# Kernel tuning notes

Hardware: AMD Instinct MI355X
Metric: run time of the kernel (lower is better)

## Reference

```python
import jax, jax.numpy as jnp
import numpy as np

DIM = 64   # model dim == d_inner (expand=1)
Hh = 64
Ww = 64
BATCH = 4
D_IN = 64
N_ST = 8   # d_state
DT_R = 4   # dt_rank = ceil(dim/16)
K = 4      # depthwise conv kernel
NB = 8     # total CrossMambaBlocks: 4 (depth=1) + 4 final cross blocks


def setup_inputs():
    key = jax.random.key(0)
    ks = iter(jax.random.split(key, 40))
    def rn(shape, s=0.02):
        return jax.random.normal(next(ks), shape, jnp.float32) * s
    A_init = jnp.log(jnp.tile(jnp.arange(1, N_ST + 1, dtype=jnp.float32), (NB, D_IN, 1)))
    return dict(
        img1=rn((BATCH, DIM, Hh, Ww), 1.0), img2=rn((BATCH, DIM, Hh, Ww), 1.0),
        img1_sum=rn((BATCH, DIM, Hh, Ww), 1.0), img2_sum=rn((BATCH, DIM, Hh, Ww), 1.0),
        norm0_w=jnp.ones((NB, DIM)), norm0_b=jnp.zeros((NB, DIM)),
        norm1_w=jnp.ones((NB, DIM)), norm1_b=jnp.zeros((NB, DIM)),
        in_w=rn((NB, 2 * D_IN, DIM)), in_b=jnp.zeros((NB, 2 * D_IN)),
        conv_w_f=rn((NB, D_IN, 1, K), 0.1), conv_b_f=jnp.zeros((NB, D_IN)),
        conv_w_b=rn((NB, D_IN, 1, K), 0.1), conv_b_b=jnp.zeros((NB, D_IN)),
        xproj_w_f=rn((NB, DT_R + 2 * N_ST, D_IN)), xproj_w_b=rn((NB, DT_R + 2 * N_ST, D_IN)),
        dtproj_w_f=rn((NB, D_IN, DT_R), 0.1), dtproj_b_f=jnp.zeros((NB, D_IN)),
        dtproj_w_b=rn((NB, D_IN, DT_R), 0.1), dtproj_b_b=jnp.zeros((NB, D_IN)),
        A_log_f=A_init, A_log_b=A_init,
        D_f=jnp.ones((NB, D_IN)), D_b=jnp.ones((NB, D_IN)),
        ln_w=jnp.ones((NB, D_IN)), ln_b=jnp.zeros((NB, D_IN)),
        mout_w=rn((NB, DIM, D_IN)), mout_b=jnp.zeros((NB, DIM)),
        fop_w=rn((DIM, 2 * DIM)), fop_b=jnp.zeros((DIM,)),
    )


def _ln(x, w, b):
    m = x.mean(-1, keepdims=True)
    v = ((x - m) ** 2).mean(-1, keepdims=True)
    return (x - m) * jax.lax.rsqrt(v + 1e-5) * w + b


def _dwconv(x, w, b):
    # x: [b,L,d], w: [d,1,K] depthwise causal conv along L
    y = jax.lax.conv_general_dilated(
        x.transpose(0, 2, 1), w, (1,), [(K - 1, 0)],
        dimension_numbers=('NCH', 'OIH', 'NCH'),
        feature_group_count=x.shape[-1])
    return y.transpose(0, 2, 1) + b


def _ssm(u, dt, Bm, Cm, A, Dm):
    # u,dt: [b,L,d]; Bm,Cm: [b,L,n]; A: [d,n]; Dm: [d]
    dA = jnp.exp(dt[..., None] * A)                 # [b,L,d,n]
    dBu = (dt * u)[..., None] * Bm[:, :, None, :]   # [b,L,d,n]
    def step(h, xs):
        dA_t, dBu_t, C_t = xs
        h = dA_t * h + dBu_t
        return h, jnp.einsum('bdn,bn->bd', h, C_t)
    h0 = jnp.zeros(u.shape[:1] + A.shape, u.dtype)
    _, ys = jax.lax.scan(step, h0, (jnp.moveaxis(dA, 1, 0), jnp.moveaxis(dBu, 1, 0), jnp.moveaxis(Cm, 1, 0)))
    return jnp.moveaxis(ys, 0, 1) + u * Dm


def _direction(x_in, extra, conv_w, conv_b, xproj_w, dtproj_w, dtproj_b, A_log, Dm, flip):
    if flip:
        x_in = x_in[:, ::-1]
        extra = extra[:, ::-1]
    u = jax.nn.silu(_dwconv(x_in, conv_w, conv_b))
    dbl = jnp.einsum('bld,ed->ble', extra, xproj_w)     # cross: dt/B/C from extra embedding
    dtr = dbl[..., :DT_R]
    Bm = dbl[..., DT_R:DT_R + N_ST]
    Cm = dbl[..., DT_R + N_ST:]
    dt = jax.nn.softplus(jnp.einsum('blr,dr->bld', dtr, dtproj_w) + dtproj_b)
    y = _ssm(u, dt, Bm, Cm, -jnp.exp(A_log), Dm)
    if flip:
        y = y[:, ::-1]
    return y


def _cross_block(i, x, extra, p):
    skip = x
    x = _ln(x, p['norm0_w'][i], p['norm0_b'][i])
    extra = _ln(extra, p['norm1_w'][i], p['norm1_b'][i])
    xz = jnp.einsum('bld,ed->ble', x, p['in_w'][i]) + p['in_b'][i]
    x_in, z = xz[..., :D_IN], xz[..., D_IN:]
    y_f = _direction(x_in, extra, p['conv_w_f'][i], p['conv_b_f'][i], p['xproj_w_f'][i],
                     p['dtproj_w_f'][i], p['dtproj_b_f'][i], p['A_log_f'][i], p['D_f'][i], False)
    y_b = _direction(x_in, extra, p['conv_w_b'][i], p['conv_b_b'][i], p['xproj_w_b'][i],
                     p['dtproj_w_b'][i], p['dtproj_b_b'][i], p['A_log_b'][i], p['D_b'][i], True)
    y = 0.5 * (y_f + y_b)                    # if_devide_out=True
    y = _ln(y, p['ln_w'][i], p['ln_b'][i])   # use_norm=True
    y = y * jax.nn.silu(z)
    out = jnp.einsum('bld,ed->ble', y, p['mout_w'][i]) + p['mout_b'][i]
    return out + skip


def _forward(img1, img2, img1_sum, img2_sum, norm0_w, norm0_b, norm1_w, norm1_b, in_w, in_b,
             conv_w_f, conv_b_f, conv_w_b, conv_b_b, xproj_w_f, xproj_w_b,
             dtproj_w_f, dtproj_b_f, dtproj_w_b, dtproj_b_b, A_log_f, A_log_b,
             D_f, D_b, ln_w, ln_b, mout_w, mout_b, fop_w, fop_b):
    p = dict(norm0_w=norm0_w, norm0_b=norm0_b, norm1_w=norm1_w, norm1_b=norm1_b,
             in_w=in_w, in_b=in_b, conv_w_f=conv_w_f, conv_b_f=conv_b_f,
             conv_w_b=conv_w_b, conv_b_b=conv_b_b, xproj_w_f=xproj_w_f, xproj_w_b=xproj_w_b,
             dtproj_w_f=dtproj_w_f, dtproj_b_f=dtproj_b_f, dtproj_w_b=dtproj_w_b,
             dtproj_b_b=dtproj_b_b, A_log_f=A_log_f, A_log_b=A_log_b, D_f=D_f, D_b=D_b,
             ln_w=ln_w, ln_b=ln_b, mout_w=mout_w, mout_b=mout_b)
    def seq(t):
        b, c, h, w = t.shape
        return t.reshape(b, c, h * w).transpose(0, 2, 1)   # b (h w) c
    s1, s2, s1s, s2s = seq(img1), seq(img2), seq(img1_sum), seq(img2_sum)
    # depth=1 cross-fusion loop
    s1 = _cross_block(0, s1, s1s, p)
    s2 = _cross_block(1, s2, s2s, p)
    s1s = _cross_block(2, s1s, s1, p)
    s2s = _cross_block(3, s2s, s2, p)
    # final cross blocks
    i1l = _cross_block(4, s1, s2, p)
    i1g = _cross_block(5, s1, s2s, p)
    i2l = _cross_block(6, s2, s1, p)
    i2g = _cross_block(7, s2, s1s, p)
    c1 = jnp.concatenate([i1l, i1g], -1)
    c2 = jnp.concatenate([i2l, i2g], -1)
    fusion = jnp.einsum('ble,ce->blc', 0.5 * (c1 + c2), fop_w) + fop_b
    b = img1.shape[0]
    return fusion.transpose(0, 2, 1).reshape(b, DIM, Hh, Ww)


def reference(img1, img2, img1_sum, img2_sum, norm0_w, norm0_b, norm1_w, norm1_b, in_w, in_b,
              conv_w_f, conv_b_f, conv_w_b, conv_b_b, xproj_w_f, xproj_w_b,
              dtproj_w_f, dtproj_b_f, dtproj_w_b, dtproj_b_b, A_log_f, A_log_b,
              D_f, D_b, ln_w, ln_b, mout_w, mout_b, fop_w, fop_b):
    return _forward(img1, img2, img1_sum, img2_sum, norm0_w, norm0_b, norm1_w, norm1_b, in_w, in_b,
                    conv_w_f, conv_b_f, conv_w_b, conv_b_b, xproj_w_f, xproj_w_b,
                    dtproj_w_f, dtproj_b_f, dtproj_w_b, dtproj_b_b, A_log_f, A_log_b,
                    D_f, D_b, ln_w, ln_b, mout_w, mout_b, fop_w, fop_b)
```

## Files before the change

kernel.cpp:

```cpp
#include <hip/hip_runtime.h>
#include <hip/hip_bf16.h>

#define BX 4
#define LX 4096
#define DX 64
#define NX 8
#define TCH 16
#define NCH 256
#define BLD (BX*LX*DX)

typedef unsigned short u16;
typedef __attribute__((ext_vector_type(8))) short v8s;
typedef __attribute__((ext_vector_type(4))) float v4f;

#define L2E 1.44269504088896f
#define LN2 0.69314718055994531f

__device__ __forceinline__ float b2f(u16 u){ return __uint_as_float(((unsigned)u)<<16); }
__device__ __forceinline__ u16 f2b(float f){
  unsigned u = __float_as_uint(f);
  unsigned r = (u + 0x7FFFu + ((u>>16)&1u)) >> 16;
  return (u16)r;
}
__device__ __forceinline__ float siluf(float x){
  return x * __builtin_amdgcn_rcpf(1.f + __builtin_amdgcn_exp2f(-x*L2E));
}
__device__ __forceinline__ float softplusf(float x){
  const float t = __builtin_amdgcn_exp2f(-fabsf(x)*L2E);
  return fmaxf(x, 0.f) + LN2 * __builtin_amdgcn_logf(1.f + t);
}

__device__ __forceinline__ v4f mfma16(v8s a, v8s b, v4f c){
  return __builtin_amdgcn_mfma_f32_16x16x32_bf16(a, b, c, 0, 0, 0);
}
__device__ __forceinline__ void split8(const float* v, v8s& hi, v8s& lo){
  #pragma unroll
  for(int j=0;j<8;j++){
    const short h = (short)f2b(v[j]);
    hi[j] = h;
    lo[j] = (short)f2b(v[j] - b2f((u16)h));
  }
}
__device__ __forceinline__ void afrag(const float* tile, int lane, int k0, v8s& hi, v8s& lo){
  const float* p = tile + (lane&15)*72 + k0 + ((lane>>4)<<3);
  float v[8];
  const float4 a = *(const float4*)(p);
  const float4 b = *(const float4*)(p+4);
  v[0]=a.x; v[1]=a.y; v[2]=a.z; v[3]=a.w;
  v[4]=b.x; v[5]=b.y; v[6]=b.z; v[7]=b.w;
  split8(v, hi, lo);
}

struct Ctx {
  const float *nw0,*nb0,*nw1,*nb1;
  const float *inb;
  const float *convw,*convb;
  const float *dtw,*dtb;
  const float *A2,*Dp;
  const float *lnw,*lnb;
  const float *moutb;
  const float *fopb;
  const u16 *wih,*wil,*wxh,*wxl,*wmh,*wml,*wfh,*wfl;
  float *act[4], *outc[4];
  float *xin[4], *zz[4], *dbl[4], *Pp[4], *qq[4], *hin[4];
};

struct BlkDesc { int i; const float* x; const float* e; float* out; int slot; };
struct StageArgs { BlkDesc d[4]; };

struct PrepEnt { const void* src; float* dst; int n; int mode; };
struct PrepAll { PrepEnt a[21]; };
struct WPrep { const void* sA; const void* sB; u16* dh; u16* dl; long off; int E; int KS; int kind; int i; };
struct WPrepAll { WPrep a[25]; };

__global__ __launch_bounds__(256) void k_prep(PrepAll pa, WPrepAll wa, const u16* df){
  const bool isbf = (df[0] == 0x3F80u);
  if(blockIdx.y < 21){
    PrepEnt p = pa.a[blockIdx.y];
    int idx = blockIdx.x*256 + threadIdx.x;
    if(idx < p.n){
      float v = isbf ? b2f(((const u16*)p.src)[idx]) : ((const float*)p.src)[idx];
      if(p.mode==2) v = -__expf(v) * L2E;
      p.dst[idx] = v;
    }
  } else {
    WPrep p = wa.a[blockIdx.y - 21];
    const int wv = threadIdx.x >> 6, lane = threadIdx.x & 63;
    const int idx = blockIdx.x*4 + wv;
    const int NT = (p.E + 15) >> 4;
    if(idx >= NT*p.KS) return;
    const int ct = idx / p.KS, ks = idx % p.KS;
    const int g  = ct*16 + (lane & 15);
    const int k0 = ks*32 + ((lane>>4)<<3);
    const int K  = p.KS*32;
    bool valid; long si = 0; const void* sp = p.sA;
    if(p.kind == 1){
      valid = (g < 40);
      const int dir = g/20, e = g - dir*20;
      if(dir) sp = p.sB;
      si = ((long)p.i*20 + e)*64 + k0;
    } else {
      valid = (g < p.E);
      si = p.off + (long)g*K + k0;
    }
    float v[8];
    #pragma unroll
    for(int j2=0;j2<8;j2++){
      float x = 0.f;
      if(valid) x = isbf ? b2f(((const u16*)sp)[si+j2]) : ((const float*)sp)[si+j2];
      v[j2] = x;
    }
    v8s hi, lo; split8(v, hi, lo);
    const size_t o = ((size_t)idx*64 + lane)*8;
    *(v8s*)(p.dh + o) = hi;
    *(v8s*)(p.dl + o) = lo;
  }
}

struct SeqArgs { const void* src[4]; };

__global__ __launch_bounds__(256) void k_seq(SeqArgs s, Ctx c, const u16* df){
  const bool isbf = (df[0] == 0x3F80u);
  __shared__ float ld[64*65];
  const int t = blockIdx.z, b = blockIdx.y, l0 = blockIdx.x*64;
  float* dst = c.act[t];
  const int tx = threadIdx.x, ty = threadIdx.y;
  if(isbf){
    const u16* src = (const u16*)s.src[t];
    #pragma unroll
    for(int k=0;k<16;k++){ int d = k*4+ty; ld[d*65+tx] = b2f(src[(size_t)(b*64+d)*LX + l0+tx]); }
  } else {
    const float* src = (const float*)s.src[t];
    #pragma unroll
    for(int k=0;k<16;k++){ int d = k*4+ty; ld[d*65+tx] = src[(size_t)(b*64+d)*LX + l0+tx]; }
  }
  __syncthreads();
  #pragma unroll
  for(int k=0;k<16;k++){ int p = k*4+ty; dst[(size_t)(b*LX + l0+p)*64 + tx] = ld[tx*65+p]; }
}

__device__ __forceinline__ void coop72(float* sb, const float* g, int t){
  #pragma unroll
  for(int k=0;k<4;k++){
    const int idx = k*256 + t;
    const int row = idx >> 4;
    const int c4  = (idx & 15) << 2;
    *(float4*)(sb + row*72 + c4) = *(const float4*)(g + (size_t)row*64 + c4);
  }
}
__device__ __forceinline__ void coop72_avg(float* sb, const float* g0, const float* g1, int t){
  #pragma unroll
  for(int k=0;k<4;k++){
    const int idx = k*256 + t;
    const int row = idx >> 4;
    const int c4  = (idx & 15) << 2;
    const float4 a = *(const float4*)(g0 + (size_t)row*64 + c4);
    const float4 b = *(const float4*)(g1 + (size_t)row*64 + c4);
    float4 o; o.x=0.5f*(a.x+b.x); o.y=0.5f*(a.y+b.y); o.z=0.5f*(a.z+b.z); o.w=0.5f*(a.w+b.w);
    *(float4*)(sb + row*72 + c4) = o;
  }
}

__device__ __forceinline__ void ln72(float* sb, int lane, const float* w, const float* b){
  float r[64];
  float* p = sb + lane*72;
  #pragma unroll
  for(int cc=0;cc<64;cc+=4){ float4 v = *(const float4*)(p+cc); r[cc]=v.x; r[cc+1]=v.y; r[cc+2]=v.z; r[cc+3]=v.w; }
  float m=0.f;
  #pragma unroll
  for(int d=0;d<64;d++) m += r[d];
  m *= (1.f/64.f);
  float va=0.f;
  #pragma unroll
  for(int d=0;d<64;d++){ float t=r[d]-m; va += t*t; }
  va *= (1.f/64.f);
  const float rs = rsqrtf(va + 1e-5f);
  #pragma unroll
  for(int d=0;d<64;d++) r[d] = (r[d]-m)*rs*w[d] + b[d];
  #pragma unroll
  for(int cc=0;cc<64;cc+=4){ float4 v={r[cc],r[cc+1],r[cc+2],r[cc+3]}; *(float4*)(p+cc)=v; }
}

__global__ __launch_bounds__(256) void k_front(Ctx c, StageArgs sa){
  __shared__ __align__(16) float sx[64*72];
  __shared__ __align__(16) float se[64*72];
  const BlkDesc bd = sa.d[blockIdx.y];
  const int i = bd.i;
  const int tile = blockIdx.x;
  const int b = tile >> 6;
  const int l0 = (tile & 63) << 6;
  const int bl0 = b*LX + l0;
  const int t = threadIdx.x;
  const int wave = t >> 6, lane = t & 63;

  coop72(sx, bd.x + (size_t)bl0*64, t);
  coop72(se, bd.e + (size_t)bl0*64, t);
  __syncthreads();
  if(wave == 0)      ln72(sx, lane, c.nw0 + i*64, c.nb0 + i*64);
  else if(wave == 1) ln72(se, lane, c.nw1 + i*64, c.nb1 + i*64);
  __syncthreads();

  const int m0 = wave*16;
  const int q  = lane >> 4;
  const int n15 = lane & 15;

  {
    v8s ah[2], al[2];
    afrag(sx + m0*72, lane, 0,  ah[0], al[0]);
    afrag(sx + m0*72, lane, 32, ah[1], al[1]);
    const v8s* WH = (const v8s*)c.wih + (size_t)i*1024;
    const v8s* WL = (const v8s*)c.wil + (size_t)i*1024;
    #pragma unroll 1
    for(int ct=0; ct<8; ct++){
      const int colg = ct*16 + n15;
      const float bias = c.inb[i*128 + colg];
      v4f acc = {bias, bias, bias, bias};
      #pragma unroll
      for(int ks=0; ks<2; ks++){
        const v8s wh = WH[(ct*2+ks)*64 + lane];
        const v8s wl = WL[(ct*2+ks)*64 + lane];
        acc = mfma16(ah[ks], wl, acc);
        acc = mfma16(al[ks], wh, acc);
        acc = mfma16(ah[ks], wh, acc);
      }
      float* baseo = (colg < 64) ? c.xin[bd.slot] : c.zz[bd.slot];
      const int col = colg & 63;
      #pragma unroll
      for(int r=0;r<4;r++){
        const int row = m0 + q*4 + r;
        baseo[(size_t)(bl0+row)*64 + col] = acc[r];
      }
    }
  }
  {
    v8s ah[2], al[2];
    afrag(se + m0*72, lane, 0,  ah[0], al[0]);
    afrag(se + m0*72, lane, 32, ah[1], al[1]);
    const v8s* WH = (const v8s*)c.wxh + (size_t)i*384;
    const v8s* WL = (const v8s*)c.wxl + (size_t)i*384;
    #pragma unroll 1
    for(int ct=0; ct<3; ct++){
      v4f acc = {0.f,0.f,0.f,0.f};
      #pragma unroll
      for(int ks=0; ks<2; ks++){
        const v8s wh = WH[(ct*2+ks)*64 + lane];
        const v8s wl = WL[(ct*2+ks)*64 + lane];
        acc = mfma16(ah[ks], wl, acc);
        acc = mfma16(al[ks], wh, acc);
        acc = mfma16(ah[ks], wh, acc);
      }
      const int g = ct*16 + n15;
      if(g < 40){
        const int dir = (g >= 20);
        const int e = g - dir*20;
        float* dp = c.dbl[bd.slot] + (size_t)dir*((size_t)BX*LX*20);
        #pragma unroll
        for(int r=0;r<4;r++){
          const int row = m0 + q*4 + r;
          dp[(size_t)(bl0+row)*20 + e] = acc[r];
        }
      }
    }
  }
}

template<int DIR>
__device__ __forceinline__ void scan1_dir(const float* xs, const float* meta,
    const float4 cwv, const float cbv, const float4 dwv, const float dtbv,
    const float* A2, float* h, float& S){
  #pragma unroll
  for(int t=0;t<TCH;t++){
    float w0,w1,w2,xc; int lr;
    if(DIR==0){ lr=t;       w0=xs[t];    w1=xs[t+1];  w2=xs[t+2];  xc=xs[t+3]; }
    else      { lr=15-t;    w0=xs[18-t]; w1=xs[17-t]; w2=xs[16-t]; xc=xs[15-t]; }
    const float u = siluf(cwv.x*w0 + cwv.y*w1 + cwv.z*w2 + cwv.w*xc + cbv);
    const float* m = meta + lr*20;
    const float4 m0 = *(const float4*)(m);
    const float dt = softplusf(m0.x*dwv.x + m0.y*dwv.y + m0.z*dwv.z + m0.w*dwv.w + dtbv);
    const float du = dt*u;
    const float4 mb0 = *(const float4*)(m+4);
    const float4 mb1 = *(const float4*)(m+8);
    const float Bv[8] = {mb0.x,mb0.y,mb0.z,mb0.w,mb1.x,mb1.y,mb1.z,mb1.w};
    #pragma unroll
    for(int n=0;n<8;n++){
      const float dA = __builtin_amdgcn_exp2f(dt*A2[n]);
      h[n] = dA*h[n] + du*Bv[n];
    }
    S += dt;
  }
}

__global__ __launch_bounds__(64) void k_scan1(Ctx c, StageArgs sa){
  __shared__ __align__(16) float meta[TCH*20];
  const int zid = blockIdx.z;
  const int j = zid >> 1, dir = zid & 1;
  const BlkDesc bd = sa.d[j];
  const int i = bd.i, slot = bd.slot;
  const int ch = blockIdx.x, b = blockIdx.y;
  const int d = threadIdx.x;
  const int pb = (dir*8 + i)*64 + d;

  const float4 cwv = *(const float4*)(c.convw + (size_t)pb*4);
  const float  cbv = c.convb[pb];
  const float4 dwv = *(const float4*)(c.dtw + (size_t)pb*4);
  const float  dtbv = c.dtb[pb];
  const float4 A2a = *(const float4*)(c.A2 + (size_t)pb*8);
  const float4 A2b = *(const float4*)(c.A2 + (size_t)pb*8 + 4);
  float A2[8] = {A2a.x,A2a.y,A2a.z,A2a.w,A2b.x,A2b.y,A2b.z,A2b.w};

  {
    const float4* s = (const float4*)(c.dbl[slot] + (size_t)dir*((size_t)BX*LX*20)
                                      + (size_t)(b*LX + ch*TCH)*20);
    float4* dst = (float4*)meta;
    #pragma unroll
    for(int k=0;k<2;k++){ int idx = k*64 + d; if(idx < 80) dst[idx] = s[idx]; }
  }
  __syncthreads();

  const int base = ch*TCH;
  const float* X = c.xin[slot] + (size_t)b*LX*64 + d;
  float xs[19];
  if(dir==0){
    #pragma unroll
    for(int k=0;k<19;k++){ const int r = base - 3 + k; xs[k] = (r>=0) ? X[(size_t)r*64] : 0.f; }
  } else {
    #pragma unroll
    for(int k=0;k<19;k++){ const int r = base + k; xs[k] = (r<LX) ? X[(size_t)r*64] : 0.f; }
  }

  float h[8];
  #pragma unroll
  for(int n=0;n<8;n++) h[n]=0.f;
  float S = 0.f;
  if(dir==0) scan1_dir<0>(xs, meta, cwv, cbv, dwv, dtbv, A2, h, S);
  else       scan1_dir<1>(xs, meta, cwv, cbv, dwv, dtbv, A2, h, S);

  float* Pw = c.Pp[slot] + (size_t)(dir*NCH + ch)*((size_t)BX*512) + (size_t)b*512 + d;
  float* Qw = c.qq[slot] + (size_t)(dir*NCH + ch)*((size_t)BX*512) + (size_t)b*512 + d;
  #pragma unroll
  for(int n=0;n<8;n++){
    Pw[n*64] = __builtin_amdgcn_exp2f(A2[n]*S);
    Qw[n*64] = h[n];
  }
}

__global__ __launch_bounds__(64) void k_mid(Ctx c, StageArgs sa){
  const int b = blockIdx.x >> 3;
  const int seg = blockIdx.x & 7;
  const int dir = blockIdx.y & 1, j = blockIdx.y >> 1;
  const BlkDesc bd = sa.d[j];
  const int slot = bd.slot;
  const int nd = seg*64 + threadIdx.x;
  const size_t base = (size_t)dir*NCH*((size_t)BX*512) + (size_t)b*512 + nd;
  const size_t STR = (size_t)BX*512;
  const float* P = c.Pp[slot] + base;
  const float* Q = c.qq[slot] + base;
  float* H = c.hin[slot] + base;
  float h = 0.f;
  float Pv[32], Qv[32];
  #pragma unroll 1
  for(int g=0; g<NCH/32; g++){
    #pragma unroll
    for(int k=0;k<32;k++){
      const int ch = dir ? (NCH-1 - (g*32+k)) : (g*32+k);
      Pv[k] = P[(size_t)ch*STR]; Qv[k] = Q[(size_t)ch*STR];
    }
    #pragma unroll
    for(int k=0;k<32;k++){
      const int ch = dir ? (NCH-1 - (g*32+k)) : (g*32+k);
      H[(size_t)ch*STR] = h;
      h = fmaf(Pv[k], h, Qv[k]);
    }
  }
}

__global__ __launch_bounds__(256) void k_back(Ctx c, StageArgs sa){
  __shared__ __align__(16) float sy[64*72];
  __shared__ __align__(16) float smeta[64*40];
  const BlkDesc bd = sa.d[blockIdx.y];
  const int i = bd.i, slot = bd.slot;
  const int tile = blockIdx.x;
  const int b = tile >> 6;
  const int l0 = (tile & 63) << 6;
  const int bl0 = b*LX + l0;
  const int t = threadIdx.x;
  const int wave = t >> 6, lane = t & 63;

  #pragma unroll
  for(int d2=0; d2<2; d2++){
    const float4* s = (const float4*)(c.dbl[slot] + (size_t)d2*((size_t)BX*LX*20) + (size_t)bl0*20);
    #pragma unroll
    for(int k=0;k<2;k++){
      const int idx = k*256 + t;
      if(idx < 320){
        const int row = idx/5, e4 = idx - row*5;
        *(float4*)(smeta + row*40 + d2*20 + e4*4) = s[idx];
      }
    }
  }
  __syncthreads();

  const int m0 = wave*16;
  {
    const int ch = (tile & 63)*4 + wave;
    const int d2 = lane;
    const float* X = c.xin[slot] + (size_t)b*LX*64 + d2;
    float xs[22];
    #pragma unroll
    for(int k=0;k<22;k++){
      const int r = l0 + m0 + k - 3;
      xs[k] = (r>=0 && r<LX) ? X[(size_t)r*64] : 0.f;
    }
    #pragma unroll
    for(int dir=0; dir<2; dir++){
      const int pb = (dir*8 + i)*64 + d2;
      const float4 cwv = *(const float4*)(c.convw + (size_t)pb*4);
      const float  cbv = c.convb[pb];
      const float4 dwv = *(const float4*)(c.dtw + (size_t)pb*4);
      const float  dtbv = c.dtb[pb];
      const float4 A2a = *(const float4*)(c.A2 + (size_t)pb*8);
      const float4 A2b = *(const float4*)(c.A2 + (size_t)pb*8 + 4);
      const float A2r[8] = {A2a.x,A2a.y,A2a.z,A2a.w,A2b.x,A2b.y,A2b.z,A2b.w};
      const float Dv = c.Dp[pb];
      float h[8];
      const float* hp = c.hin[slot] + (size_t)(dir*NCH + ch)*((size_t)BX*512) + (size_t)b*512 + d2;
      #pragma unroll
      for(int n=0;n<8;n++) h[n] = hp[n*64];
      #pragma unroll
      for(int k=0;k<16;k++){
        const int lr = dir ? (m0+15-k) : (m0+k);
        const float w0 = dir ? xs[21-k] : xs[k];
        const float w1 = dir ? xs[20-k] : xs[k+1];
        const float w2 = dir ? xs[19-k] : xs[k+2];
        const float xc = dir ? xs[18-k] : xs[k+3];
        const float u = siluf(cwv.x*w0 + cwv.y*w1 + cwv.z*w2 + cwv.w*xc + cbv);
        const float* m = smeta + lr*40 + dir*20;
        const float4 m0v = *(const float4*)(m);
        const float dt = softplusf(m0v.x*dwv.x + m0v.y*dwv.y + m0v.z*dwv.z + m0v.w*dwv.w + dtbv);
        const float du = dt*u;
        const float4 mb0 = *(const float4*)(m+4);
        const float4 mb1 = *(const float4*)(m+8);
        const float Bv[8] = {mb0.x,mb0.y,mb0.z,mb0.w,mb1.x,mb1.y,mb1.z,mb1.w};
        float yv = u*Dv;
        #pragma unroll
        for(int n=0;n<8;n++){
          const float dA = __builtin_amdgcn_exp2f(dt*A2r[n]);
          h[n] = dA*h[n] + du*Bv[n];
        }
        const float4 mc0 = *(const float4*)(m+12);
        const float4 mc1 = *(const float4*)(m+16);
        const float Cv[8] = {mc0.x,mc0.y,mc0.z,mc0.w,mc1.x,mc1.y,mc1.z,mc1.w};
        #pragma unroll
        for(int n=0;n<8;n++) yv += h[n]*Cv[n];
        if(dir==0) sy[lr*72 + d2] = 0.5f*yv;
        else       sy[lr*72 + d2] += 0.5f*yv;
      }
    }
  }
  __syncthreads();
  if(wave == 0){
    ln72(sy, lane, c.lnw + i*64, c.lnb + i*64);
    float* p = sy + lane*72;
    const float* zp = c.zz[slot] + (size_t)(bl0+lane)*64;
    #pragma unroll
    for(int d3=0;d3<64;d3++){ p[d3] *= siluf(zp[d3]); }
  }
  __syncthreads();

  const int q  = lane >> 4;
  const int n15 = lane & 15;
  v8s ah[2], al[2];
  afrag(sy + m0*72, lane, 0,  ah[0], al[0]);
  afrag(sy + m0*72, lane, 32, ah[1], al[1]);
  const v8s* WH = (const v8s*)c.wmh + (size_t)i*512;
  const v8s* WL = (const v8s*)c.wml + (size_t)i*512;
  #pragma unroll 1
  for(int ct=0; ct<4; ct++){
    const int col = ct*16 + n15;
    const float bias = c.moutb[i*64 + col];
    v4f acc = {bias, bias, bias, bias};
    #pragma unroll
    for(int ks=0; ks<2; ks++){
      const v8s wh = WH[(ct*2+ks)*64 + lane];
      const v8s wl = WL[(ct*2+ks)*64 + lane];
      acc = mfma16(ah[ks], wl, acc);
      acc = mfma16(al[ks], wh, acc);
      acc = mfma16(ah[ks], wh, acc);
    }
    #pragma unroll
    for(int r=0;r<4;r++){
      const int row = m0 + q*4 + r;
      bd.out[(size_t)(bl0+row)*64 + col] = acc[r] + bd.x[(size_t)(bl0+row)*64 + col];
    }
  }
}

__global__ __launch_bounds__(256) void k_fusion(Ctx c, void* outp, const u16* df){
  const bool isbf = (df[0] == 0x3F80u);
  __shared__ __align__(16) float sL[64*72];
  __shared__ __align__(16) float sH[64*72];
  __shared__ __align__(16) float sT[64*68];
  const int tile = blockIdx.x;
  const int b = tile >> 6;
  const int l0 = (tile & 63) << 6;
  const int bl0 = b*LX + l0;
  const int t = threadIdx.x;
  const int wave = t >> 6, lane = t & 63;

  coop72_avg(sL, c.outc[0] + (size_t)bl0*64, c.outc[2] + (size_t)bl0*64, t);
  coop72_avg(sH, c.outc[1] + (size_t)bl0*64, c.outc[3] + (size_t)bl0*64, t);
  __syncthreads();

  const int m0 = wave*16;
  const int q  = lane >> 4;
  const int n15 = lane & 15;
  v8s ah[4], al[4];
  afrag(sL + m0*72, lane, 0,  ah[0], al[0]);
  afrag(sL + m0*72, lane, 32, ah[1], al[1]);
  afrag(sH + m0*72, lane, 0,  ah[2], al[2]);
  afrag(sH + m0*72, lane, 32, ah[3], al[3]);
  const v8s* WH = (const v8s*)c.wfh;
  const v8s* WL = (const v8s*)c.wfl;
  #pragma unroll 1
  for(int ct=0; ct<4; ct++){
    const int col = ct*16 + n15;
    const float bias = c.fopb[col];
    v4f acc = {bias, bias, bias, bias};
    #pragma unroll
    for(int ks=0; ks<4; ks++){
      const v8s wh = WH[(ct*4+ks)*64 + lane];
      const v8s wl = WL[(ct*4+ks)*64 + lane];
      acc = mfma16(ah[ks], wl, acc);
      acc = mfma16(al[ks], wh, acc);
      acc = mfma16(ah[ks], wh, acc);
    }
    #pragma unroll
    for(int r=0;r<4;r++) sT[col*68 + m0 + q*4 + r] = acc[r];
  }
  __syncthreads();

  const int o  = t >> 2;
  const int p0 = (t & 3) * 16;
  float v[16];
  #pragma unroll
  for(int k=0;k<16;k+=4){
    const float4 x = *(const float4*)(sT + o*68 + p0 + k);
    v[k]=x.x; v[k+1]=x.y; v[k+2]=x.z; v[k+3]=x.w;
  }
  const size_t off = (size_t)(b*64+o)*LX + l0 + p0;
  if(isbf){
    u16 hb[16];
    #pragma unroll
    for(int k=0;k<16;k++) hb[k] = f2b(v[k]);
    uint4 u0, u1;
    u0.x = hb[0] | ((unsigned)hb[1]<<16);  u0.y = hb[2] | ((unsigned)hb[3]<<16);
    u0.z = hb[4] | ((unsigned)hb[5]<<16);  u0.w = hb[6] | ((unsigned)hb[7]<<16);
    u1.x = hb[8] | ((unsigned)hb[9]<<16);  u1.y = hb[10]| ((unsigned)hb[11]<<16);
    u1.z = hb[12]| ((unsigned)hb[13]<<16); u1.w = hb[14]| ((unsigned)hb[15]<<16);
    *(uint4*)((u16*)outp + off)     = u0;
    *(uint4*)((u16*)outp + off + 8) = u1;
  } else {
    float* fo = (float*)outp + off;
    #pragma unroll
    for(int k=0;k<16;k+=4){ float4 x={v[k],v[k+1],v[k+2],v[k+3]}; *(float4*)(fo+k)=x; }
  }
}

extern "C" void kernel_launch(void* const* d_in, const int* in_sizes, int n_in,
                              void* d_out, int out_size, void* d_ws, size_t ws_size,
                              hipStream_t stream){
  (void)in_sizes; (void)out_size;
  if(n_in < 30) return;
  const u16* df = (const u16*)d_in[22];
  float* w = (float*)d_ws;
  size_t off = 0;
  auto al = [&](size_t n){ float* p = w + off; off += n; return p; };

  Ctx c;
  float* nw0 = al(512);  float* nb0 = al(512);
  float* nw1 = al(512);  float* nb1 = al(512);
  float* inb = al(1024);
  float* convw = al(4096); float* convb = al(1024);
  float* dtw = al(4096); float* dtb = al(1024);
  float* A2 = al(8192);  float* Dp = al(1024);
  float* lnw = al(512);  float* lnb = al(512);
  float* moutb = al(512);
  float* fopb = al(64);
  c.nw0=nw0; c.nb0=nb0; c.nw1=nw1; c.nb1=nb1;
  c.inb=inb; c.convw=convw; c.convb=convb;
  c.dtw=dtw; c.dtb=dtb; c.A2=A2; c.Dp=Dp;
  c.lnw=lnw; c.lnb=lnb; c.moutb=moutb; c.fopb=fopb;

  u16* wih = (u16*)al(32768); u16* wil = (u16*)al(32768);
  u16* wxh = (u16*)al(12288); u16* wxl = (u16*)al(12288);
  u16* wmh = (u16*)al(16384); u16* wml = (u16*)al(16384);
  u16* wfh = (u16*)al(4096);  u16* wfl = (u16*)al(4096);
  c.wih=wih; c.wil=wil; c.wxh=wxh; c.wxl=wxl; c.wmh=wmh; c.wml=wml; c.wfh=wfh; c.wfl=wfl;

  for(int k=0;k<4;k++) c.act[k]  = al(BLD);
  for(int k=0;k<4;k++) c.outc[k] = al(BLD);

  const size_t CHW = 2*(size_t)NCH*BX*512;
  const size_t SLOT = (size_t)BLD + BLD + 2*(size_t)BX*LX*20 + 3*CHW;
  const size_t avail = ws_size/4;
  int nslots = 4;
  while(nslots>1 && off + (size_t)nslots*SLOT > avail) nslots >>= 1;
  for(int s=0;s<nslots;s++){
    c.xin[s]=al(BLD); c.zz[s]=al(BLD); c.dbl[s]=al(2*(size_t)BX*LX*20);
    c.Pp[s]=al(CHW); c.qq[s]=al(CHW); c.hin[s]=al(CHW);
  }
  for(int s=nslots;s<4;s++){
    c.xin[s]=c.xin[0]; c.zz[s]=c.zz[0]; c.dbl[s]=c.dbl[0];
    c.Pp[s]=c.Pp[0]; c.qq[s]=c.qq[0]; c.hin[s]=c.hin[0];
  }

  PrepAll pa;
  int kk = 0;
  auto add = [&](int idx, float* dst, int n, int mode){
    pa.a[kk].src=d_in[idx]; pa.a[kk].dst=dst; pa.a[kk].n=n; pa.a[kk].mode=mode; kk++;
  };
  add(4,  nw0, 512, 0); add(5,  nb0, 512, 0);
  add(6,  nw1, 512, 0); add(7,  nb1, 512, 0);
  add(9,  inb, 1024, 0);
  add(10, convw, 2048, 0);      add(11, convb, 512, 0);
  add(12, convw+2048, 2048, 0); add(13, convb+512, 512, 0);
  add(16, dtw, 2048, 0);        add(17, dtb, 512, 0);
  add(18, dtw+2048, 2048, 0);   add(19, dtb+512, 512, 0);
  add(20, A2, 4096, 2);         add(21, A2+4096, 4096, 2);
  add(22, Dp, 512, 0);          add(23, Dp+512, 512, 0);
  add(24, lnw, 512, 0);         add(25, lnb, 512, 0);
  add(27, moutb, 512, 0);
  add(29, fopb, 64, 0);

  WPrepAll wa;
  for(int i=0;i<8;i++) wa.a[i]    = { d_in[8],  nullptr,  wih+(size_t)i*8192, wil+(size_t)i*8192, (long)i*8192, 128, 2, 0, i };
  for(int i=0;i<8;i++) wa.a[8+i]  = { d_in[14], d_in[15], wxh+(size_t)i*3072, wxl+(size_t)i*3072, 0,            48, 2, 1, i };
  for(int i=0;i<8;i++) wa.a[16+i] = { d_in[26], nullptr,  wmh+(size_t)i*4096, wml+(size_t)i*4096, (long)i*4096, 64, 2, 0, i };
  wa.a[24] = { d_in[28], nullptr, wfh, wfl, 0, 64, 4, 0, 0 };

  k_prep<<<dim3(16,46),256,0,stream>>>(pa, wa, df);

  SeqArgs sq;
  for(int t=0;t<4;t++) sq.src[t] = d_in[t];
  k_seq<<<dim3(64,BX,4), dim3(64,4), 0, stream>>>(sq, c, df);

  BlkDesc R1[2] = {{0, c.act[0], c.act[2], c.act[0], 0},
                   {1, c.act[1], c.act[3], c.act[1], 0}};
  BlkDesc R2[4] = {{2, c.act[2], c.act[0], c.act[2], 0},
                   {3, c.act[3], c.act[1], c.act[3], 0},
                   {4, c.act[0], c.act[1], c.outc[0], 0},
                   {6, c.act[1], c.act[0], c.outc[2], 0}};
  BlkDesc R3[2] = {{5, c.act[0], c.act[3], c.outc[1], 0},
                   {7, c.act[1], c.act[2], c.outc[3], 0}};

  auto run = [&](BlkDesc* ds, int cnt){
    for(int k=0;k<cnt;k+=nslots){
      int n = cnt-k; if(n>nslots) n = nslots;
      StageArgs sa;
      for(int j=0;j<n;j++){ sa.d[j] = ds[k+j]; sa.d[j].slot = j; }
      for(int j=n;j<4;j++) sa.d[j] = sa.d[0];
      k_front<<<dim3(256,n),      256, 0, stream>>>(c, sa);
      k_scan1<<<dim3(NCH,BX,2*n),  64, 0, stream>>>(c, sa);
      k_mid  <<<dim3(BX*8,2*n),    64, 0, stream>>>(c, sa);
      k_back <<<dim3(256,n),      256, 0, stream>>>(c, sa);
    }
  };
  run(R1,2); run(R2,4); run(R3,2);
  k_fusion<<<256,256,0,stream>>>(c, d_out, df);
}
```

Before: 352.7 us.

## Merge input transpose into prep kernel and prefetch in-proj weights

Folds the k_seq NCHW-to-BLD transpose into k_prep as extra grid rows, which saves one kernel launch. In k_front, the in-proj weight fragments are prefetched one column-tile ahead so their global loads overlap the MFMA work. The z-gating load becomes float4 vectorised, and several small GEMM loops now have unroll pragmas. The price is more register pressure and a larger prep kernel that reserves shared memory on every block.

```diff
diff --git a/kernel.cpp b/kernel.cpp
--- a/kernel.cpp
+++ b/kernel.cpp
@@ -67,24 +67,27 @@
 
 struct BlkDesc { int i; const float* x; const float* e; float* out; int slot; };
 struct StageArgs { BlkDesc d[4]; };
+struct SeqArgs { const void* src[4]; };
 
 struct PrepEnt { const void* src; float* dst; int n; int mode; };
 struct PrepAll { PrepEnt a[21]; };
 struct WPrep { const void* sA; const void* sB; u16* dh; u16* dl; long off; int E; int KS; int kind; int i; };
 struct WPrepAll { WPrep a[25]; };
 
-__global__ __launch_bounds__(256) void k_prep(PrepAll pa, WPrepAll wa, const u16* df){
+__global__ __launch_bounds__(256) void k_prep(PrepAll pa, WPrepAll wa, SeqArgs sq, Ctx c, const u16* df){
   const bool isbf = (df[0] == 0x3F80u);
-  if(blockIdx.y < 21){
-    PrepEnt p = pa.a[blockIdx.y];
+  __shared__ float ld[64*65];
+  const int y = blockIdx.y;
+  if(y < 21){
+    PrepEnt p = pa.a[y];
     int idx = blockIdx.x*256 + threadIdx.x;
     if(idx < p.n){
       float v = isbf ? b2f(((const u16*)p.src)[idx]) : ((const float*)p.src)[idx];
       if(p.mode==2) v = -__expf(v) * L2E;
       p.dst[idx] = v;
     }
-  } else {
-    WPrep p = wa.a[blockIdx.y - 21];
+  } else if(y < 46){
+    WPrep p = wa.a[y - 21];
     const int wv = threadIdx.x >> 6, lane = threadIdx.x & 63;
     const int idx = blockIdx.x*4 + wv;
     const int NT = (p.E + 15) >> 4;
@@ -114,29 +117,24 @@
     const size_t o = ((size_t)idx*64 + lane)*8;
     *(v8s*)(p.dh + o) = hi;
     *(v8s*)(p.dl + o) = lo;
-  }
-}
-
-struct SeqArgs { const void* src[4]; };
-
-__global__ __launch_bounds__(256) void k_seq(SeqArgs s, Ctx c, const u16* df){
-  const bool isbf = (df[0] == 0x3F80u);
-  __shared__ float ld[64*65];
-  const int t = blockIdx.z, b = blockIdx.y, l0 = blockIdx.x*64;
-  float* dst = c.act[t];
-  const int tx = threadIdx.x, ty = threadIdx.y;
-  if(isbf){
-    const u16* src = (const u16*)s.src[t];
-    #pragma unroll
-    for(int k=0;k<16;k++){ int d = k*4+ty; ld[d*65+tx] = b2f(src[(size_t)(b*64+d)*LX + l0+tx]); }
   } else {
-    const float* src = (const float*)s.src[t];
-    #pragma unroll
-    for(int k=0;k<16;k++){ int d = k*4+ty; ld[d*65+tx] = src[(size_t)(b*64+d)*LX + l0+tx]; }
-  }
-  __syncthreads();
-  #pragma unroll
-  for(int k=0;k<16;k++){ int p = k*4+ty; dst[(size_t)(b*LX + l0+p)*64 + tx] = ld[tx*65+p]; }
+    const int sid = (y - 46)*16 + blockIdx.x;
+    const int t4 = sid >> 8, b = (sid >> 6) & 3, l0 = (sid & 63)*64;
+    float* dst = c.act[t4];
+    const int tx = threadIdx.x & 63, ty = threadIdx.x >> 6;
+    if(isbf){
+      const u16* src = (const u16*)sq.src[t4];
+      #pragma unroll
+      for(int k=0;k<16;k++){ int d = k*4+ty; ld[d*65+tx] = b2f(src[(size_t)(b*64+d)*LX + l0+tx]); }
+    } else {
+      const float* src = (const float*)sq.src[t4];
+      #pragma unroll
+      for(int k=0;k<16;k++){ int d = k*4+ty; ld[d*65+tx] = src[(size_t)(b*64+d)*LX + l0+tx]; }
+    }
+    __syncthreads();
+    #pragma unroll
+    for(int k=0;k<16;k++){ int p = k*4+ty; dst[(size_t)(b*LX + l0+p)*64 + tx] = ld[tx*65+p]; }
+  }
 }
 
 __device__ __forceinline__ void coop72(float* sb, const float* g, int t){
@@ -198,6 +196,11 @@
   __syncthreads();
   if(wave == 0)      ln72(sx, lane, c.nw0 + i*64, c.nb0 + i*64);
   else if(wave == 1) ln72(se, lane, c.nw1 + i*64, c.nb1 + i*64);
+
+  const v8s* WH = (const v8s*)c.wih + (size_t)i*1024;
+  const v8s* WL = (const v8s*)c.wil + (size_t)i*1024;
+  v8s cwh0 = WH[lane],     cwh1 = WH[64 + lane];
+  v8s cwl0 = WL[lane],     cwl1 = WL[64 + lane];
   __syncthreads();
 
   const int m0 = wave*16;
@@ -208,21 +211,22 @@
     v8s ah[2], al[2];
     afrag(sx + m0*72, lane, 0,  ah[0], al[0]);
     afrag(sx + m0*72, lane, 32, ah[1], al[1]);
-    const v8s* WH = (const v8s*)c.wih + (size_t)i*1024;
-    const v8s* WL = (const v8s*)c.wil + (size_t)i*1024;
     #pragma unroll 1
     for(int ct=0; ct<8; ct++){
+      v8s nwh0, nwh1, nwl0, nwl1;
+      if(ct < 7){
+        nwh0 = WH[((ct+1)*2+0)*64 + lane]; nwh1 = WH[((ct+1)*2+1)*64 + lane];
+        nwl0 = WL[((ct+1)*2+0)*64 + lane]; nwl1 = WL[((ct+1)*2+1)*64 + lane];
+      }
       const int colg = ct*16 + n15;
       const float bias = c.inb[i*128 + colg];
       v4f acc = {bias, bias, bias, bias};
-      #pragma unroll
-      for(int ks=0; ks<2; ks++){
-        const v8s wh = WH[(ct*2+ks)*64 + lane];
-        const v8s wl = WL[(ct*2+ks)*64 + lane];
-        acc = mfma16(ah[ks], wl, acc);
-        acc = mfma16(al[ks], wh, acc);
-        acc = mfma16(ah[ks], wh, acc);
-      }
+      acc = mfma16(ah[0], cwl0, acc);
+      acc = mfma16(al[0], cwh0, acc);
+      acc = mfma16(ah[0], cwh0, acc);
+      acc = mfma16(ah[1], cwl1, acc);
+      acc = mfma16(al[1], cwh1, acc);
+      acc = mfma16(ah[1], cwh1, acc);
       float* baseo = (colg < 64) ? c.xin[bd.slot] : c.zz[bd.slot];
       const int col = colg & 63;
       #pragma unroll
@@ -230,21 +234,22 @@
         const int row = m0 + q*4 + r;
         baseo[(size_t)(bl0+row)*64 + col] = acc[r];
       }
+      cwh0 = nwh0; cwh1 = nwh1; cwl0 = nwl0; cwl1 = nwl1;
     }
   }
   {
     v8s ah[2], al[2];
     afrag(se + m0*72, lane, 0,  ah[0], al[0]);
     afrag(se + m0*72, lane, 32, ah[1], al[1]);
-    const v8s* WH = (const v8s*)c.wxh + (size_t)i*384;
-    const v8s* WL = (const v8s*)c.wxl + (size_t)i*384;
-    #pragma unroll 1
+    const v8s* XH = (const v8s*)c.wxh + (size_t)i*384;
+    const v8s* XL = (const v8s*)c.wxl + (size_t)i*384;
+    #pragma unroll
     for(int ct=0; ct<3; ct++){
       v4f acc = {0.f,0.f,0.f,0.f};
       #pragma unroll
       for(int ks=0; ks<2; ks++){
-        const v8s wh = WH[(ct*2+ks)*64 + lane];
-        const v8s wl = WL[(ct*2+ks)*64 + lane];
+        const v8s wh = XH[(ct*2+ks)*64 + lane];
+        const v8s wl = XL[(ct*2+ks)*64 + lane];
         acc = mfma16(ah[ks], wl, acc);
         acc = mfma16(al[ks], wh, acc);
         acc = mfma16(ah[ks], wh, acc);
@@ -461,9 +466,13 @@
   if(wave == 0){
     ln72(sy, lane, c.lnw + i*64, c.lnb + i*64);
     float* p = sy + lane*72;
-    const float* zp = c.zz[slot] + (size_t)(bl0+lane)*64;
-    #pragma unroll
-    for(int d3=0;d3<64;d3++){ p[d3] *= siluf(zp[d3]); }
+    const float4* zp = (const float4*)(c.zz[slot] + (size_t)(bl0+lane)*64);
+    #pragma unroll
+    for(int d3=0;d3<16;d3++){
+      const float4 z4 = zp[d3];
+      p[d3*4+0] *= siluf(z4.x); p[d3*4+1] *= siluf(z4.y);
+      p[d3*4+2] *= siluf(z4.z); p[d3*4+3] *= siluf(z4.w);
+    }
   }
   __syncthreads();
 
@@ -474,7 +483,7 @@
   afrag(sy + m0*72, lane, 32, ah[1], al[1]);
   const v8s* WH = (const v8s*)c.wmh + (size_t)i*512;
   const v8s* WL = (const v8s*)c.wml + (size_t)i*512;
-  #pragma unroll 1
+  #pragma unroll
   for(int ct=0; ct<4; ct++){
     const int col = ct*16 + n15;
     const float bias = c.moutb[i*64 + col];
@@ -521,7 +530,7 @@
   afrag(sH + m0*72, lane, 32, ah[3], al[3]);
   const v8s* WH = (const v8s*)c.wfh;
   const v8s* WL = (const v8s*)c.wfl;
-  #pragma unroll 1
+  #pragma unroll 2
   for(int ct=0; ct<4; ct++){
     const int col = ct*16 + n15;
     const float bias = c.fopb[col];
@@ -638,11 +647,10 @@
   for(int i=0;i<8;i++) wa.a[16+i] = { d_in[26], nullptr,  wmh+(size_t)i*4096, wml+(size_t)i*4096, (long)i*4096, 64, 2, 0, i };
   wa.a[24] = { d_in[28], nullptr, wfh, wfl, 0, 64, 4, 0, 0 };
 
-  k_prep<<<dim3(16,46),256,0,stream>>>(pa, wa, df);
-
   SeqArgs sq;
   for(int t=0;t<4;t++) sq.src[t] = d_in[t];
-  k_seq<<<dim3(64,BX,4), dim3(64,4), 0, stream>>>(sq, c, df);
+
+  k_prep<<<dim3(16,110),256,0,stream>>>(pa, wa, sq, c, df);
 
   BlkDesc R1[2] = {{0, c.act[0], c.act[2], c.act[0], 0},
                    {1, c.act[1], c.act[3], c.act[1], 0}};
```

Measured after the change: 344.7 us. 1.02x faster.
